# Kernel optimization log

Measured on AMD Instinct MI355X. Metric: run time of the kernel, lower is better.

Reference implementation:

```python
import jax, jax.numpy as jnp
import numpy as np

HIDDEN = 2048
N_HEADS = 16
HEAD_DIM = 128
N_EXPERTS = 8
TOP_K = 2
INTER = 1024
EPS = 1e-5
ROPE_THETA = 10000.0
T = 2048


def rms_norm(x, w, eps=EPS):
    xf = x.astype(jnp.float32)
    return (xf * jax.lax.rsqrt(jnp.mean(xf * xf, axis=-1, keepdims=True) + eps)).astype(x.dtype) * w


def apply_rope(x, positions):
    # x: [T, H, D], NeoX-style half rotation
    d = x.shape[-1]
    inv_freq = 1.0 / (ROPE_THETA ** (jnp.arange(0, d, 2, dtype=jnp.float32) / d))
    ang = positions.astype(jnp.float32)[:, None] * inv_freq  # [T, D/2]
    cos = jnp.cos(ang)[:, None, :]
    sin = jnp.sin(ang)[:, None, :]
    x1, x2 = jnp.split(x, 2, axis=-1)
    return jnp.concatenate([x1 * cos - x2 * sin, x2 * cos + x1 * sin], axis=-1)


def setup_inputs() -> dict:
    key = jax.random.key(0)
    ks = jax.random.split(key, 8)
    s = 0.02
    return {
        "positions": jnp.arange(T, dtype=jnp.int32),
        "hidden_states": jax.random.normal(ks[0], (T, HIDDEN), jnp.float32),
        "qkv_w": jax.random.normal(ks[1], (3 * HIDDEN, HIDDEN), jnp.float32) * s,
        "o_w": jax.random.normal(ks[2], (HIDDEN, HIDDEN), jnp.float32) * s,
        "q_norm_w": jnp.ones((N_HEADS * HEAD_DIM,), jnp.float32),
        "k_norm_w": jnp.ones((N_HEADS * HEAD_DIM,), jnp.float32),
        "post_attn_norm_w": jnp.ones((HIDDEN,), jnp.float32),
        "post_ffn_norm_w": jnp.ones((HIDDEN,), jnp.float32),
        "gate_w": jax.random.normal(ks[3], (N_EXPERTS, HIDDEN), jnp.float32) * s,
        "w_gate": jax.random.normal(ks[4], (N_EXPERTS, INTER, HIDDEN), jnp.float32) * s,
        "w_up": jax.random.normal(ks[5], (N_EXPERTS, INTER, HIDDEN), jnp.float32) * s,
        "w_down": jax.random.normal(ks[6], (N_EXPERTS, HIDDEN, INTER), jnp.float32) * s,
    }


def attention(positions, x, qkv_w, o_w, q_norm_w, k_norm_w):
    qkv = x @ qkv_w.T  # [T, 3*HIDDEN]
    q, k, v = jnp.split(qkv, 3, axis=-1)
    q = rms_norm(q, q_norm_w)  # norm over full flat q dim (FlexOlmo/OLMoE style)
    k = rms_norm(k, k_norm_w)
    q = apply_rope(q.reshape(T, N_HEADS, HEAD_DIM), positions)
    k = apply_rope(k.reshape(T, N_HEADS, HEAD_DIM), positions)
    v = v.reshape(T, N_HEADS, HEAD_DIM)
    scale = 1.0 / np.sqrt(HEAD_DIM)
    scores = jnp.einsum('thd,shd->hts', q, k) * scale
    mask = jnp.tril(jnp.ones((T, T), bool))
    scores = jnp.where(mask[None], scores, -jnp.inf)
    p = jax.nn.softmax(scores, axis=-1)
    out = jnp.einsum('hts,shd->thd', p, v).reshape(T, HIDDEN)
    return out @ o_w.T


def moe(x, gate_w, w_gate, w_up, w_down):
    logits = (x @ gate_w.T).astype(jnp.float32)  # router_logits.float()
    probs = jax.nn.softmax(logits, axis=-1)
    topv, topi = jax.lax.top_k(probs, TOP_K)  # renormalize=False -> use raw softmax weights
    # dense per-expert combine weights: [T, E]
    wdense = jnp.zeros((T, N_EXPERTS), jnp.float32)
    wdense = jnp.sum(jax.nn.one_hot(topi, N_EXPERTS, dtype=jnp.float32) * topv[..., None], axis=1)
    # detach().clone() before dispatch (inference semantics: value unchanged)
    xe = jax.lax.stop_gradient(x)
    g = jnp.einsum('td,efd->tef', xe, w_gate)
    u = jnp.einsum('td,efd->tef', xe, w_up)
    h = jax.nn.silu(g) * u
    y = jnp.einsum('tef,edf->ted', h, w_down)
    return jnp.einsum('ted,te->td', y, wdense)


def reference(positions, hidden_states, qkv_w, o_w, q_norm_w, k_norm_w,
              post_attn_norm_w, post_ffn_norm_w, gate_w, w_gate, w_up, w_down):
    residual = hidden_states
    h = attention(positions, hidden_states, qkv_w, o_w, q_norm_w, k_norm_w)
    h = rms_norm(h, post_attn_norm_w)
    h = h + residual
    residual = h
    h = moe(h, gate_w, w_gate, w_up, w_down)
    h = rms_norm(h, post_ffn_norm_w)
    return residual + h
```

## Files before the change

kernel.cpp:

```cpp
#include <hip/hip_runtime.h>
#include <hip/hip_bf16.h>
#include <cmath>

#define TT 2048
#define HID 2048
#define NHEADS 16
#define HDIM 128
#define NEXP 8
#define INTERD 1024
#define EPSV 1e-5f

typedef short bf16x8 __attribute__((ext_vector_type(8)));
typedef float f32x4 __attribute__((ext_vector_type(4)));

__device__ __forceinline__ unsigned short f2bf(float f) {
    unsigned int u = __builtin_bit_cast(unsigned int, f);
    unsigned int r = (u + 0x7FFFu + ((u >> 16) & 1u)) >> 16;
    return (unsigned short)r;
}
__device__ __forceinline__ float bf2f(unsigned short h) {
    return __builtin_bit_cast(float, (unsigned int)h << 16);
}

__device__ __forceinline__ void gll16(const void* g, void* l) {
    __builtin_amdgcn_global_load_lds((const __attribute__((address_space(1))) void*)g,
                                     (__attribute__((address_space(3))) void*)l, 16, 0, 0);
}

__device__ __forceinline__ float block_reduce_sum_256(float v, float* red) {
    const int tid = threadIdx.x;
    red[tid] = v;
    __syncthreads();
    for (int s = 128; s > 0; s >>= 1) {
        if (tid < s) red[tid] += red[tid + s];
        __syncthreads();
    }
    float r = red[0];
    __syncthreads();
    return r;
}

__global__ __launch_bounds__(256) void split_f32k(const float* __restrict__ x,
                                                  unsigned short* __restrict__ hi,
                                                  unsigned short* __restrict__ lo, int n4) {
    int i = blockIdx.x * 256 + threadIdx.x;
    if (i >= n4) return;
    float4 v = reinterpret_cast<const float4*>(x)[i];
    float xs[4] = {v.x, v.y, v.z, v.w};
    unsigned short hs[4], ls[4];
#pragma unroll
    for (int u = 0; u < 4; ++u) {
        hs[u] = f2bf(xs[u]);
        ls[u] = f2bf(xs[u] - bf2f(hs[u]));
    }
    uint2 hp; hp.x = hs[0] | ((unsigned)hs[1] << 16); hp.y = hs[2] | ((unsigned)hs[3] << 16);
    uint2 lp; lp.x = ls[0] | ((unsigned)ls[1] << 16); lp.y = ls[2] | ((unsigned)ls[3] << 16);
    *reinterpret_cast<uint2*>(hi + (size_t)i * 4) = hp;
    *reinterpret_cast<uint2*>(lo + (size_t)i * 4) = lp;
}

__global__ __launch_bounds__(256) void cvt_bf(const float* __restrict__ x,
                                              unsigned short* __restrict__ y, int n4) {
    int i = blockIdx.x * 256 + threadIdx.x;
    if (i >= n4) return;
    float4 v = reinterpret_cast<const float4*>(x)[i];
    uint2 p;
    p.x = (unsigned)f2bf(v.x) | ((unsigned)f2bf(v.y) << 16);
    p.y = (unsigned)f2bf(v.z) | ((unsigned)f2bf(v.w) << 16);
    *reinterpret_cast<uint2*>(y + (size_t)i * 4) = p;
}

#define GSTAGE(BUF, K0)                                                             \
    {                                                                               \
        char* base_ = (char*)Smem + (BUF) * 32768;                                  \
        _Pragma("unroll")                                                           \
        for (int i_ = 0; i_ < 2; ++i_) {                                            \
            int c_ = tid + i_ * 256;                                                \
            int r_ = c_ >> 2, s_ = c_ & 3;                                          \
            int ko_ = (K0) + (((s_ ^ ((r_ >> 1) & 3)) & 3) << 3);                   \
            gll16(Ah + (size_t)(m0 + r_) * lda + ko_, base_ + c_ * 16);             \
            gll16(Al + (size_t)(m0 + r_) * lda + ko_, base_ + 8192 + c_ * 16);      \
            gll16(Bh + (size_t)(n0 + r_) * K + ko_, base_ + 16384 + c_ * 16);       \
            gll16(Bl + (size_t)(n0 + r_) * K + ko_, base_ + 24576 + c_ * 16);       \
        }                                                                           \
    }

__global__ __launch_bounds__(256) void gemm_sp(const unsigned short* __restrict__ Ah,
                                               const unsigned short* __restrict__ Al,
                                               const unsigned short* __restrict__ Bh,
                                               const unsigned short* __restrict__ Bl,
                                               float* __restrict__ C, int N, int K, int lda) {
    const int nbx = gridDim.x;
    const int nwg = nbx * gridDim.y;
    const int orig = blockIdx.y * nbx + blockIdx.x;
    const int qq = nwg >> 3, rr = nwg & 7;
    const int xcd = orig & 7, loc = orig >> 3;
    const int wgid = (xcd < rr ? xcd * (qq + 1) : rr * (qq + 1) + (xcd - rr) * qq) + loc;
    const int m0 = (wgid / nbx) * 128, n0 = (wgid % nbx) * 128;

    __shared__ __align__(16) unsigned short Smem[2 * 4 * 128 * 32];
    const int tid = threadIdx.x;
    const int w = tid >> 6, l = tid & 63;
    const int lr = l & 15, lg = l >> 4;
    const int wm = w >> 1, wn = w & 1;

    f32x4 acc[4][4];
#pragma unroll
    for (int i = 0; i < 4; ++i)
#pragma unroll
        for (int j = 0; j < 4; ++j) acc[i][j] = f32x4{0.f, 0.f, 0.f, 0.f};

    const int nks = K >> 5;
    GSTAGE(0, 0);
    int cur = 0;
    for (int ks = 0; ks < nks; ++ks) {
        if (ks + 1 < nks) {
            GSTAGE(cur ^ 1, (ks + 1) << 5);
            asm volatile("s_waitcnt vmcnt(8)" ::: "memory");
        } else {
            asm volatile("s_waitcnt vmcnt(0)" ::: "memory");
        }
        __builtin_amdgcn_s_barrier();
        __builtin_amdgcn_sched_barrier(0);
        char* bb = (char*)Smem + cur * 32768;
        bf16x8 bhf[4], blf[4];
#pragma unroll
        for (int nt = 0; nt < 4; ++nt) {
            int row = wn * 64 + nt * 16 + lr;
            int off = row * 64 + (((lg ^ ((row >> 1) & 3)) & 3) << 4);
            bhf[nt] = *reinterpret_cast<const bf16x8*>(bb + 16384 + off);
            blf[nt] = *reinterpret_cast<const bf16x8*>(bb + 24576 + off);
        }
        __builtin_amdgcn_s_setprio(1);
#pragma unroll
        for (int mt = 0; mt < 4; ++mt) {
            int row = wm * 64 + mt * 16 + lr;
            int off = row * 64 + (((lg ^ ((row >> 1) & 3)) & 3) << 4);
            bf16x8 ahf = *reinterpret_cast<const bf16x8*>(bb + off);
            bf16x8 alf = *reinterpret_cast<const bf16x8*>(bb + 8192 + off);
#pragma unroll
            for (int nt = 0; nt < 4; ++nt) {
                acc[mt][nt] = __builtin_amdgcn_mfma_f32_16x16x32_bf16(ahf, bhf[nt], acc[mt][nt], 0, 0, 0);
                acc[mt][nt] = __builtin_amdgcn_mfma_f32_16x16x32_bf16(ahf, blf[nt], acc[mt][nt], 0, 0, 0);
                acc[mt][nt] = __builtin_amdgcn_mfma_f32_16x16x32_bf16(alf, bhf[nt], acc[mt][nt], 0, 0, 0);
            }
        }
        __builtin_amdgcn_s_setprio(0);
        asm volatile("s_waitcnt lgkmcnt(0)" ::: "memory");
        __builtin_amdgcn_s_barrier();
        __builtin_amdgcn_sched_barrier(0);
        cur ^= 1;
    }
#pragma unroll
    for (int mt = 0; mt < 4; ++mt) {
#pragma unroll
        for (int r = 0; r < 4; ++r) {
            size_t crow = (size_t)(m0 + wm * 64 + mt * 16 + lg * 4 + r) * N;
#pragma unroll
            for (int nt = 0; nt < 4; ++nt)
                C[crow + n0 + wn * 64 + nt * 16 + lr] = acc[mt][nt][r];
        }
    }
}

#define GSTAGE_BF(BUF, K0)                                                           \
    {                                                                                \
        char* base_ = sm + (BUF) * 16384;                                            \
        int ko_ = (K0) + x0s;                                                        \
        gll16(A + arow0 * lda + ko_, base_ + tid * 16);                              \
        gll16(A + arow1 * lda + ko_, base_ + (tid + 256) * 16);                      \
        gll16(Bp + brow0 * K + ko_, base_ + 8192 + tid * 16);                        \
        gll16(Bp + brow1 * K + ko_, base_ + 8192 + (tid + 256) * 16);                \
    }

template<int MODE>
__global__ __launch_bounds__(256) void gemm_bf(const unsigned short* __restrict__ A,
                                               const unsigned short* __restrict__ B,
                                               void* __restrict__ Cout,
                                               const float* __restrict__ gsrc,
                                               int N, int K, int lda,
                                               size_t strideB,
                                               const int* __restrict__ gather,
                                               const int* __restrict__ offs,
                                               const int* __restrict__ counts) {
    const int e = blockIdx.z;
    const int cnt = counts[e];
    const int base = offs[e];
    const int m0 = blockIdx.y * 128;
    if (m0 >= cnt) return;
    const int n0 = blockIdx.x * 128;
    const unsigned short* Bp = B + (size_t)e * strideB;

    __shared__ __align__(16) unsigned short Smem[2 * 2 * 128 * 32];
    char* sm = (char*)Smem;
    const int tid = threadIdx.x;
    const int w = tid >> 6, l = tid & 63;
    const int lr = l & 15, lg = l >> 4;
    const int wm = w >> 1, wn = w & 1;

    const int r0 = tid >> 2, s0 = tid & 3;
    const int r1 = r0 + 64;
    const int x0s = ((s0 ^ ((r0 >> 1) & 3)) & 3) << 3;
    const size_t arow0 = (size_t)gather[base + min(m0 + r0, cnt - 1)];
    const size_t arow1 = (size_t)gather[base + min(m0 + r1, cnt - 1)];
    const size_t brow0 = (size_t)(n0 + r0);
    const size_t brow1 = (size_t)(n0 + r1);

    f32x4 acc[4][4];
#pragma unroll
    for (int i = 0; i < 4; ++i)
#pragma unroll
        for (int j = 0; j < 4; ++j) acc[i][j] = f32x4{0.f, 0.f, 0.f, 0.f};

    const int nks = K >> 5;
    GSTAGE_BF(0, 0);
    int cur = 0;
    for (int ks = 0; ks < nks; ++ks) {
        if (ks + 1 < nks) {
            GSTAGE_BF(cur ^ 1, (ks + 1) << 5);
            asm volatile("s_waitcnt vmcnt(4)" ::: "memory");
        } else {
            asm volatile("s_waitcnt vmcnt(0)" ::: "memory");
        }
        __builtin_amdgcn_s_barrier();
        __builtin_amdgcn_sched_barrier(0);
        char* bb = sm + cur * 16384;
        bf16x8 bfr[4];
#pragma unroll
        for (int nt = 0; nt < 4; ++nt) {
            int row = wn * 64 + nt * 16 + lr;
            int off = row * 64 + (((lg ^ ((row >> 1) & 3)) & 3) << 4);
            bfr[nt] = *reinterpret_cast<const bf16x8*>(bb + 8192 + off);
        }
        __builtin_amdgcn_s_setprio(1);
#pragma unroll
        for (int mt = 0; mt < 4; ++mt) {
            int row = wm * 64 + mt * 16 + lr;
            int off = row * 64 + (((lg ^ ((row >> 1) & 3)) & 3) << 4);
            bf16x8 af = *reinterpret_cast<const bf16x8*>(bb + off);
#pragma unroll
            for (int nt = 0; nt < 4; ++nt)
                acc[mt][nt] = __builtin_amdgcn_mfma_f32_16x16x32_bf16(af, bfr[nt], acc[mt][nt], 0, 0, 0);
        }
        __builtin_amdgcn_s_setprio(0);
        asm volatile("s_waitcnt lgkmcnt(0)" ::: "memory");
        __builtin_amdgcn_s_barrier();
        __builtin_amdgcn_sched_barrier(0);
        cur ^= 1;
    }
#pragma unroll
    for (int mt = 0; mt < 4; ++mt) {
#pragma unroll
        for (int r = 0; r < 4; ++r) {
            int rowl = wm * 64 + mt * 16 + lg * 4 + r;
            if (m0 + rowl < cnt) {
                size_t crow = (size_t)(base + m0 + rowl) * N;
#pragma unroll
                for (int nt = 0; nt < 4; ++nt) {
                    size_t idx = crow + n0 + wn * 64 + nt * 16 + lr;
                    if (MODE == 1) {
                        float g = gsrc[idx];
                        ((unsigned short*)Cout)[idx] = f2bf(g / (1.f + expf(-g)) * acc[mt][nt][r]);
                    } else {
                        ((float*)Cout)[idx] = acc[mt][nt][r];
                    }
                }
            }
        }
    }
}

__global__ __launch_bounds__(256) void gemm_moe_down(const unsigned short* __restrict__ Abf,
                                                     const float* __restrict__ B,
                                                     float* __restrict__ C,
                                                     int N, int K, int lda,
                                                     size_t strideB,
                                                     const int* __restrict__ offs,
                                                     const int* __restrict__ counts) {
    const int e = blockIdx.z;
    const int cnt = counts[e];
    const int base = offs[e];
    const int m0 = blockIdx.y * 128;
    if (m0 >= cnt) return;
    const int n0 = blockIdx.x * 128;
    const float* Bp = B + (size_t)e * strideB;

    __shared__ unsigned short smA[128 * 64];
    __shared__ unsigned short smB[128 * 64];
    const int tid = threadIdx.x;
    const int w = tid >> 6, l = tid & 63;
    const int lr = l & 15, lg = l >> 4;
    const int wm = w >> 1, wn = w & 1;
    char* sA = (char*)smA;
    char* sB = (char*)smB;

    f32x4 acc[4][4];
#pragma unroll
    for (int i = 0; i < 4; ++i)
#pragma unroll
        for (int j = 0; j < 4; ++j) acc[i][j] = f32x4{0.f, 0.f, 0.f, 0.f};

    for (int k0 = 0; k0 < K; k0 += 64) {
#pragma unroll
        for (int i = 0; i < 4; ++i) {
            int slot = tid + i * 256;
            int r = slot >> 3, sg = slot & 7;
            int arow = base + min(m0 + r, cnt - 1);
            uint4 v = *reinterpret_cast<const uint4*>(&Abf[(size_t)arow * lda + k0 + sg * 8]);
            *reinterpret_cast<uint4*>(sA + r * 128 + ((sg * 16) ^ ((r & 7) << 4))) = v;
        }
#pragma unroll
        for (int i = 0; i < 8; ++i) {
            int slot = tid + i * 256;
            int r = slot >> 4, kq = slot & 15;
            float4 bv = *reinterpret_cast<const float4*>(&Bp[(size_t)(n0 + r) * K + k0 + kq * 4]);
            uint2 pk;
            pk.x = (unsigned)f2bf(bv.x) | ((unsigned)f2bf(bv.y) << 16);
            pk.y = (unsigned)f2bf(bv.z) | ((unsigned)f2bf(bv.w) << 16);
            *reinterpret_cast<uint2*>(sB + r * 128 + ((kq * 8) ^ ((r & 7) << 4))) = pk;
        }
        __syncthreads();
#pragma unroll
        for (int kk = 0; kk < 2; ++kk) {
            bf16x8 af[4], bfr[4];
#pragma unroll
            for (int mt = 0; mt < 4; ++mt) {
                int row = wm * 64 + mt * 16 + lr;
                af[mt] = *reinterpret_cast<const bf16x8*>(sA + row * 128 + ((kk * 64 + lg * 16) ^ ((row & 7) << 4)));
            }
#pragma unroll
            for (int nt = 0; nt < 4; ++nt) {
                int row = wn * 64 + nt * 16 + lr;
                bfr[nt] = *reinterpret_cast<const bf16x8*>(sB + row * 128 + ((kk * 64 + lg * 16) ^ ((row & 7) << 4)));
            }
#pragma unroll
            for (int mt = 0; mt < 4; ++mt)
#pragma unroll
                for (int nt = 0; nt < 4; ++nt)
                    acc[mt][nt] = __builtin_amdgcn_mfma_f32_16x16x32_bf16(af[mt], bfr[nt], acc[mt][nt], 0, 0, 0);
        }
        __syncthreads();
    }
#pragma unroll
    for (int mt = 0; mt < 4; ++mt) {
#pragma unroll
        for (int r = 0; r < 4; ++r) {
            int rowl = wm * 64 + mt * 16 + lg * 4 + r;
            if (m0 + rowl < cnt) {
                size_t crow = (size_t)(base + m0 + rowl) * N;
#pragma unroll
                for (int nt = 0; nt < 4; ++nt)
                    C[crow + n0 + wn * 64 + nt * 16 + lr] = acc[mt][nt][r];
            }
        }
    }
}

__global__ __launch_bounds__(256) void qknorm_rope_split(float* __restrict__ qkv,
                                                         const float* __restrict__ qw,
                                                         const float* __restrict__ kw,
                                                         const int* __restrict__ pos) {
    __shared__ float xbuf[2048];
    __shared__ float red[256];
    const int t = blockIdx.x, tid = threadIdx.x;
    unsigned short* row16 = (unsigned short*)(qkv + (size_t)t * 6144);
    const float pf = (float)pos[t];
    float vreg[8];
    const float* vsrc = qkv + (size_t)t * 6144 + 4096;
#pragma unroll
    for (int i = 0; i < 8; ++i) vreg[i] = vsrc[tid + i * 256];
    __syncthreads();
#pragma unroll
    for (int i = 0; i < 8; ++i) {
        int d = tid + i * 256;
        unsigned short hi = f2bf(vreg[i]);
        row16[8192 + d] = hi;
        row16[10240 + d] = f2bf(vreg[i] - bf2f(hi));
    }
    for (int part = 0; part < 2; ++part) {
        const float* x = qkv + (size_t)t * 6144 + part * 2048;
        const float* wn = part ? kw : qw;
        const int sbase = part ? 4096 : 0;
        const float outscale = part ? 1.0f : 0.08838834764831845f;
        float s = 0.f;
#pragma unroll
        for (int i = 0; i < 8; ++i) {
            int d = tid + i * 256;
            float v = x[d];
            xbuf[d] = v;
            s = fmaf(v, v, s);
        }
        float tot = block_reduce_sum_256(s, red);
        float scale = rsqrtf(tot * (1.f / HID) + EPSV);
#pragma unroll
        for (int p = tid; p < 1024; p += 256) {
            int hh = p >> 6, j = p & 63;
            int i1 = hh * 128 + j, i2 = i1 + 64;
            float x1 = xbuf[i1] * scale * wn[i1];
            float x2 = xbuf[i2] * scale * wn[i2];
            float invf = expf(-(float)j * 0.14391156831212787f);
            float ang = pf * invf;
            float sn, cs;
            sincosf(ang, &sn, &cs);
            float o1 = (x1 * cs - x2 * sn) * outscale;
            float o2 = (x2 * cs + x1 * sn) * outscale;
            unsigned short h1_ = f2bf(o1);
            row16[sbase + i1] = h1_;
            row16[sbase + 2048 + i1] = f2bf(o1 - bf2f(h1_));
            unsigned short h2_ = f2bf(o2);
            row16[sbase + i2] = h2_;
            row16[sbase + 2048 + i2] = f2bf(o2 - bf2f(h2_));
        }
        __syncthreads();
    }
}

__global__ __launch_bounds__(256) void kvprep(const unsigned short* __restrict__ qkv16,
                                              unsigned short* __restrict__ kt,
                                              unsigned short* __restrict__ vt) {
    const int C = blockIdx.x;
    const int h = blockIdx.y;
    const int tid = threadIdx.x;
#pragma unroll
    for (int p = 0; p < 2; ++p) {
#pragma unroll
        for (int i = 0; i < 4; ++i) {
            int slot = tid + i * 256;
            int r = slot >> 4, sg = slot & 15;
            uint4 v = *reinterpret_cast<const uint4*>(
                qkv16 + (size_t)(C * 64 + r) * 12288 + 4096 + p * 2048 + h * 128 + (sg ^ (r & 7)) * 8);
            *reinterpret_cast<uint4*>(kt + (size_t)(h * 32 + C) * 16384 + p * 8192 + slot * 8) = v;
        }
    }
    __shared__ unsigned short tile[64 * 128];
    char* tb = (char*)tile;
    for (int p = 0; p < 2; ++p) {
#pragma unroll
        for (int i = 0; i < 4; ++i) {
            int c = tid + i * 256;
            int r = c >> 4, dseg = c & 15;
            uint4 v = *reinterpret_cast<const uint4*>(
                qkv16 + (size_t)(C * 64 + r) * 12288 + 8192 + p * 2048 + h * 128 + dseg * 8);
            int swz = dseg ^ (r & 7) ^ (r >> 3);
            *reinterpret_cast<uint4*>(tb + r * 256 + swz * 16) = v;
        }
        __syncthreads();
        unsigned short* ob = vt + (size_t)(h * 32 + C) * 16384 + p * 8192;
#pragma unroll
        for (int i = 0; i < 4; ++i) {
            int c = tid + i * 256;
            int d = c >> 3, j = c & 7;
            unsigned short tmp[8];
#pragma unroll
            for (int u = 0; u < 8; ++u) {
                int s = 8 * j + u;
                int swz = (d >> 3) ^ (s & 7) ^ (s >> 3);
                tmp[u] = *reinterpret_cast<const unsigned short*>(tb + s * 256 + swz * 16 + (d & 7) * 2);
            }
            *reinterpret_cast<uint4*>(ob + (size_t)d * 64 + ((j ^ (d & 7)) * 8)) =
                *reinterpret_cast<const uint4*>(tmp);
        }
        __syncthreads();
    }
}

#define STAGE1(CIDX)                                                                   \
    {                                                                                  \
        const unsigned short* kb_ = kt + (size_t)(h * 32 + (CIDX)) * 16384;            \
        const unsigned short* vb_ = vt + (size_t)(h * 32 + (CIDX)) * 16384;            \
        _Pragma("unroll")                                                              \
        for (int p_ = 0; p_ < 2; ++p_) {                                               \
            _Pragma("unroll")                                                          \
            for (int i_ = 0; i_ < 4; ++i_) {                                           \
                int slot_ = tid + i_ * 256;                                            \
                gll16(kb_ + p_ * 8192 + slot_ * 8, kvb + p_ * 16384 + slot_ * 16);     \
                gll16(vb_ + p_ * 8192 + slot_ * 8, kvb + 32768 + p_ * 16384 + slot_ * 16); \
            }                                                                          \
        }                                                                              \
    }

__global__ __launch_bounds__(256) void attn_mfma(const unsigned short* __restrict__ qkv16,
                                                 const unsigned short* __restrict__ kt,
                                                 const unsigned short* __restrict__ vt,
                                                 unsigned short* __restrict__ oh,
                                                 unsigned short* __restrict__ ol) {
    const int g = blockIdx.x;
    const int rank = (g < 256) ? g : 767 - g;
    const int h = rank & 15;
    const int t0 = (31 - (rank >> 4)) * 64;
    const int tid = threadIdx.x;
    const int w = tid >> 6, l = tid & 63;
    const int lr = l & 15, lg = l >> 4;
    const size_t RS = 12288;
    __shared__ __align__(16) unsigned short KVs[32768];
    __shared__ unsigned short Ps[4][2 * 16 * 64];
    char* kvb = (char*)KVs;
    char* PsB = (char*)(Ps[w]);

    bf16x8 qh[4], ql[4];
    {
        const unsigned short* qp = qkv16 + (size_t)(t0 + w * 16 + lr) * RS + h * 128 + lg * 8;
#pragma unroll
        for (int kk = 0; kk < 4; ++kk) {
            qh[kk] = *reinterpret_cast<const bf16x8*>(qp + kk * 32);
            ql[kk] = *reinterpret_cast<const bf16x8*>(qp + 2048 + kk * 32);
        }
    }
    f32x4 oacc[8];
#pragma unroll
    for (int dt = 0; dt < 8; ++dt) oacc[dt] = f32x4{0.f, 0.f, 0.f, 0.f};
    float mrun[4] = {-INFINITY, -INFINITY, -INFINITY, -INFINITY};
    float lrun[4] = {0.f, 0.f, 0.f, 0.f};

    for (int s0 = 0; s0 <= t0; s0 += 64) {
        STAGE1(s0 >> 6);
        __syncthreads();
        char* KsB = kvb;
        char* VtB = kvb + 32768;

        f32x4 sc[4];
#pragma unroll
        for (int nt = 0; nt < 4; ++nt) sc[nt] = f32x4{0.f, 0.f, 0.f, 0.f};
        __builtin_amdgcn_s_setprio(1);
#pragma unroll
        for (int kk = 0; kk < 4; ++kk) {
#pragma unroll
            for (int nt = 0; nt < 4; ++nt) {
                int row = nt * 16 + lr;
                int off = row * 256 + ((kk * 64 + lg * 16) ^ ((row & 7) << 4));
                bf16x8 kh = *reinterpret_cast<const bf16x8*>(KsB + off);
                bf16x8 kl = *reinterpret_cast<const bf16x8*>(KsB + 16384 + off);
                sc[nt] = __builtin_amdgcn_mfma_f32_16x16x32_bf16(qh[kk], kh, sc[nt], 0, 0, 0);
                sc[nt] = __builtin_amdgcn_mfma_f32_16x16x32_bf16(ql[kk], kh, sc[nt], 0, 0, 0);
                sc[nt] = __builtin_amdgcn_mfma_f32_16x16x32_bf16(qh[kk], kl, sc[nt], 0, 0, 0);
            }
        }
        __builtin_amdgcn_s_setprio(0);
        float mnew[4], alpha[4], psum[4];
#pragma unroll
        for (int r = 0; r < 4; ++r) {
            int row_t = t0 + w * 16 + lg * 4 + r;
            float mx = mrun[r];
#pragma unroll
            for (int nt = 0; nt < 4; ++nt) {
                int col = s0 + nt * 16 + lr;
                float v = sc[nt][r];
                if (col > row_t) v = -INFINITY;
                sc[nt][r] = v;
                mx = fmaxf(mx, v);
            }
#pragma unroll
            for (int o = 1; o < 16; o <<= 1) mx = fmaxf(mx, __shfl_xor(mx, o));
            mnew[r] = mx;
            alpha[r] = expf(mrun[r] - mx);
            mrun[r] = mx;
            psum[r] = 0.f;
        }
#pragma unroll
        for (int nt = 0; nt < 4; ++nt) {
#pragma unroll
            for (int r = 0; r < 4; ++r) {
                float p = expf(sc[nt][r] - mnew[r]);
                psum[r] += p;
                int prow = lg * 4 + r;
                int off = prow * 128 + (((nt * 16 + lr) * 2) ^ ((prow & 7) << 4));
                unsigned short ph = f2bf(p);
                *reinterpret_cast<unsigned short*>(PsB + off) = ph;
                *reinterpret_cast<unsigned short*>(PsB + 2048 + off) = f2bf(p - bf2f(ph));
            }
        }
#pragma unroll
        for (int r = 0; r < 4; ++r) {
            float s = psum[r];
#pragma unroll
            for (int o = 1; o < 16; o <<= 1) s += __shfl_xor(s, o);
            lrun[r] = lrun[r] * alpha[r] + s;
        }
#pragma unroll
        for (int dt = 0; dt < 8; ++dt)
#pragma unroll
            for (int r = 0; r < 4; ++r) oacc[dt][r] *= alpha[r];
        bf16x8 ph[2], pl[2];
#pragma unroll
        for (int kk = 0; kk < 2; ++kk) {
            int off = lr * 128 + ((kk * 64 + lg * 16) ^ ((lr & 7) << 4));
            ph[kk] = *reinterpret_cast<const bf16x8*>(PsB + off);
            pl[kk] = *reinterpret_cast<const bf16x8*>(PsB + 2048 + off);
        }
        __builtin_amdgcn_s_setprio(1);
#pragma unroll
        for (int dt = 0; dt < 8; ++dt) {
            int row = dt * 16 + lr;
#pragma unroll
            for (int kk = 0; kk < 2; ++kk) {
                int off = row * 128 + ((kk * 64 + lg * 16) ^ ((row & 7) << 4));
                bf16x8 vh = *reinterpret_cast<const bf16x8*>(VtB + off);
                bf16x8 vl = *reinterpret_cast<const bf16x8*>(VtB + 16384 + off);
                oacc[dt] = __builtin_amdgcn_mfma_f32_16x16x32_bf16(ph[kk], vh, oacc[dt], 0, 0, 0);
                oacc[dt] = __builtin_amdgcn_mfma_f32_16x16x32_bf16(ph[kk], vl, oacc[dt], 0, 0, 0);
                oacc[dt] = __builtin_amdgcn_mfma_f32_16x16x32_bf16(pl[kk], vh, oacc[dt], 0, 0, 0);
            }
        }
        __builtin_amdgcn_s_setprio(0);
        __syncthreads();
    }
#pragma unroll
    for (int r = 0; r < 4; ++r) {
        float inv = 1.f / lrun[r];
        int row_t = t0 + w * 16 + lg * 4 + r;
#pragma unroll
        for (int dt = 0; dt < 8; ++dt) {
            float o = oacc[dt][r] * inv;
            unsigned short hb = f2bf(o);
            size_t idx = (size_t)row_t * 2048 + h * 128 + dt * 16 + lr;
            oh[idx] = hb;
            ol[idx] = f2bf(o - bf2f(hb));
        }
    }
}

__global__ __launch_bounds__(256) void add_rmsnorm(const float* __restrict__ resid,
                                                   const float* __restrict__ x,
                                                   const float* __restrict__ w,
                                                   float* __restrict__ out,
                                                   unsigned short* __restrict__ outbf) {
    __shared__ float red[256];
    const int t = blockIdx.x, tid = threadIdx.x;
    const float* xr = x + (size_t)t * HID;
    float v[8];
    float s = 0.f;
#pragma unroll
    for (int i = 0; i < 8; ++i) { v[i] = xr[tid + i * 256]; s = fmaf(v[i], v[i], s); }
    float tot = block_reduce_sum_256(s, red);
    float scale = rsqrtf(tot * (1.f / HID) + EPSV);
#pragma unroll
    for (int i = 0; i < 8; ++i) {
        int d = tid + i * 256;
        float o = resid[(size_t)t * HID + d] + v[i] * scale * w[d];
        out[(size_t)t * HID + d] = o;
        outbf[(size_t)t * HID + d] = f2bf(o);
    }
}

__global__ __launch_bounds__(64) void router_kernel(const float* __restrict__ h1,
                                                    const float* __restrict__ gate_w,
                                                    int* __restrict__ topi, float* __restrict__ topv,
                                                    int* __restrict__ slot_tk, int* __restrict__ counts) {
    const int t = blockIdx.x, lane = threadIdx.x;
    float acc[NEXP] = {};
    const float* x = h1 + (size_t)t * HID;
    for (int d = lane; d < HID; d += 64) {
        float xv = x[d];
#pragma unroll
        for (int e = 0; e < NEXP; ++e) acc[e] = fmaf(xv, gate_w[e * HID + d], acc[e]);
    }
#pragma unroll
    for (int e = 0; e < NEXP; ++e)
#pragma unroll
        for (int off = 32; off > 0; off >>= 1) acc[e] += __shfl_down(acc[e], off);
    if (lane == 0) {
        float mx = acc[0];
        for (int e = 1; e < NEXP; ++e) mx = fmaxf(mx, acc[e]);
        float p[NEXP], se = 0.f;
        for (int e = 0; e < NEXP; ++e) { p[e] = expf(acc[e] - mx); se += p[e]; }
        float inv = 1.f / se;
        for (int e = 0; e < NEXP; ++e) p[e] *= inv;
        int e1 = 0;
        for (int e = 1; e < NEXP; ++e) if (p[e] > p[e1]) e1 = e;
        int e2 = (e1 == 0) ? 1 : 0;
        for (int e = 0; e < NEXP; ++e) if (e != e1 && p[e] > p[e2]) e2 = e;
        topi[t * 2] = e1;     topv[t * 2] = p[e1];
        topi[t * 2 + 1] = e2; topv[t * 2 + 1] = p[e2];
        slot_tk[t * 2]     = atomicAdd(&counts[e1], 1);
        slot_tk[t * 2 + 1] = atomicAdd(&counts[e2], 1);
    }
}

__global__ void scan_kernel(const int* __restrict__ counts, int* __restrict__ offs) {
    int o = 0;
    for (int e = 0; e < NEXP; ++e) { offs[e] = o; o += counts[e]; }
}

__global__ __launch_bounds__(256) void map_kernel(const int* __restrict__ topi,
                                                  const int* __restrict__ slot_tk,
                                                  const int* __restrict__ offs,
                                                  int* __restrict__ token_of_row,
                                                  int* __restrict__ row_of_tk) {
    int idx = blockIdx.x * 256 + threadIdx.x;
    if (idx >= TT * 2) return;
    int e = topi[idx];
    int row = offs[e] + slot_tk[idx];
    token_of_row[row] = idx >> 1;
    row_of_tk[idx] = row;
}

__global__ __launch_bounds__(256) void final_combine(const float* __restrict__ h1,
                                                     const float* __restrict__ ypart,
                                                     const float* __restrict__ topv,
                                                     const int* __restrict__ row_of_tk,
                                                     const float* __restrict__ wffn,
                                                     float* __restrict__ out) {
    __shared__ float red[256];
    const int t = blockIdx.x, tid = threadIdx.x;
    const int r0 = row_of_tk[t * 2], r1 = row_of_tk[t * 2 + 1];
    const float w0 = topv[t * 2], w1 = topv[t * 2 + 1];
    const float* y0 = ypart + (size_t)r0 * HID;
    const float* y1 = ypart + (size_t)r1 * HID;
    float v[8];
    float s = 0.f;
#pragma unroll
    for (int i = 0; i < 8; ++i) {
        int d = tid + i * 256;
        v[i] = w0 * y0[d] + w1 * y1[d];
        s = fmaf(v[i], v[i], s);
    }
    float tot = block_reduce_sum_256(s, red);
    float scale = rsqrtf(tot * (1.f / HID) + EPSV);
#pragma unroll
    for (int i = 0; i < 8; ++i) {
        int d = tid + i * 256;
        out[(size_t)t * HID + d] = h1[(size_t)t * HID + d] + v[i] * scale * wffn[d];
    }
}

extern "C" void kernel_launch(void* const* d_in, const int* in_sizes, int n_in,
                              void* d_out, int out_size, void* d_ws, size_t ws_size,
                              hipStream_t stream) {
    const int*   positions = (const int*)d_in[0];
    const float* hidden    = (const float*)d_in[1];
    const float* qkv_w     = (const float*)d_in[2];
    const float* o_w       = (const float*)d_in[3];
    const float* q_norm_w  = (const float*)d_in[4];
    const float* k_norm_w  = (const float*)d_in[5];
    const float* post_attn = (const float*)d_in[6];
    const float* post_ffn  = (const float*)d_in[7];
    const float* gate_w    = (const float*)d_in[8];
    const float* w_gate    = (const float*)d_in[9];
    const float* w_up      = (const float*)d_in[10];
    const float* w_down    = (const float*)d_in[11];
    float* out = (float*)d_out;

    char* ws = (char*)d_ws;
    size_t off = 0;
    auto alloc = [&](size_t bytes) -> void* {
        void* p = ws + off;
        off += (bytes + 255) & ~(size_t)255;
        return p;
    };
    float*          qkvbuf = (float*)alloc((size_t)TT * 6144 * 4);
    unsigned short* hidsp  = (unsigned short*)alloc((size_t)TT * HID * 2 * 2);
    unsigned short* wsp    = (unsigned short*)alloc(((size_t)6144 * HID * 2 + (size_t)HID * HID * 2) * 2);
    float*          h1     = (float*)alloc((size_t)TT * HID * 4);
    unsigned short* h1bf   = (unsigned short*)alloc((size_t)TT * HID * 2);
    int*   topi   = (int*)alloc(TT * 2 * 4);
    float* topv   = (float*)alloc(TT * 2 * 4);
    int*   slot   = (int*)alloc(TT * 2 * 4);
    int*   rowtk  = (int*)alloc(TT * 2 * 4);
    int*   tokrow = (int*)alloc(TT * 2 * 4);
    int*   counts = (int*)alloc(8 * 4);
    int*   offsb  = (int*)alloc(8 * 4);
    if (off > ws_size) return;

    unsigned short* hid_hi   = hidsp;
    unsigned short* hid_lo   = hidsp + (size_t)TT * HID;
    unsigned short* attnO_hi = hid_hi;
    unsigned short* attnO_lo = hid_lo;
    unsigned short* qkvw_hi = wsp;
    unsigned short* qkvw_lo = wsp + (size_t)6144 * HID;
    unsigned short* ow_hi   = wsp + (size_t)2 * 6144 * HID;
    unsigned short* ow_lo   = ow_hi + (size_t)HID * HID;
    unsigned short* vtbuf   = wsp;
    unsigned short* ktbuf   = wsp + (size_t)TT * HID * 2;
    unsigned short* wbfg = wsp;
    unsigned short* wbfu = wsp + (size_t)NEXP * INTERD * HID;
    float*          gbuf   = qkvbuf;
    unsigned short* hinter = (unsigned short*)(qkvbuf + (size_t)4096 * INTERD);
    float*          oOut   = qkvbuf + (size_t)8192 * INTERD;
    float*          ypart  = oOut;

    hipMemsetAsync(counts, 0, 8 * sizeof(int), stream);

    dim3 b256(256);
    split_f32k<<<dim3(TT * HID / 4 / 256), b256, 0, stream>>>(hidden, hid_hi, hid_lo, TT * HID / 4);
    split_f32k<<<dim3(6144 * HID / 4 / 256), b256, 0, stream>>>(qkv_w, qkvw_hi, qkvw_lo, 6144 * HID / 4);
    split_f32k<<<dim3(HID * HID / 4 / 256), b256, 0, stream>>>(o_w, ow_hi, ow_lo, HID * HID / 4);
    gemm_sp<<<dim3(6144 / 128, TT / 128), b256, 0, stream>>>(hid_hi, hid_lo, qkvw_hi, qkvw_lo,
                                                             qkvbuf, 6144, HID, HID);
    qknorm_rope_split<<<dim3(TT), b256, 0, stream>>>(qkvbuf, q_norm_w, k_norm_w, positions);
    kvprep<<<dim3(32, NHEADS), b256, 0, stream>>>((const unsigned short*)qkvbuf, ktbuf, vtbuf);
    attn_mfma<<<dim3(512), b256, 0, stream>>>((const unsigned short*)qkvbuf, ktbuf, vtbuf,
                                              attnO_hi, attnO_lo);
    gemm_sp<<<dim3(HID / 128, TT / 128), b256, 0, stream>>>(attnO_hi, attnO_lo, ow_hi, ow_lo,
                                                            oOut, HID, HID, HID);
    cvt_bf<<<dim3(16384), b256, 0, stream>>>(w_gate, wbfg, NEXP * INTERD * HID / 4);
    cvt_bf<<<dim3(16384), b256, 0, stream>>>(w_up,   wbfu, NEXP * INTERD * HID / 4);
    add_rmsnorm<<<dim3(TT), b256, 0, stream>>>(hidden, oOut, post_attn, h1, h1bf);
    router_kernel<<<dim3(TT), dim3(64), 0, stream>>>(h1, gate_w, topi, topv, slot, counts);
    scan_kernel<<<1, 1, 0, stream>>>(counts, offsb);
    map_kernel<<<dim3((TT * 2 + 255) / 256), b256, 0, stream>>>(topi, slot, offsb, tokrow, rowtk);
    gemm_bf<0><<<dim3(INTERD / 128, 32, NEXP), b256, 0, stream>>>(
        h1bf, wbfg, gbuf, nullptr, INTERD, HID, HID, (size_t)INTERD * HID, tokrow, offsb, counts);
    gemm_bf<1><<<dim3(INTERD / 128, 32, NEXP), b256, 0, stream>>>(
        h1bf, wbfu, hinter, gbuf, INTERD, HID, HID, (size_t)INTERD * HID, tokrow, offsb, counts);
    gemm_moe_down<<<dim3(HID / 128, 32, NEXP), b256, 0, stream>>>(
        hinter, w_down, ypart, HID, INTERD, INTERD, (size_t)HID * INTERD, offsb, counts);
    final_combine<<<dim3(TT), b256, 0, stream>>>(h1, ypart, topv, rowtk, post_ffn, out);
}
```

Before: 717.7 us.

## Fuse gate and up expert GEMMs with in-kernel fp32-to-bf16 weight conversion

New measurement: 733.0 us. 1.02x slower.

```diff
diff --git a/kernel.cpp b/kernel.cpp
--- a/kernel.cpp
+++ b/kernel.cpp
@@ -57,17 +57,6 @@
     uint2 lp; lp.x = ls[0] | ((unsigned)ls[1] << 16); lp.y = ls[2] | ((unsigned)ls[3] << 16);
     *reinterpret_cast<uint2*>(hi + (size_t)i * 4) = hp;
     *reinterpret_cast<uint2*>(lo + (size_t)i * 4) = lp;
-}
-
-__global__ __launch_bounds__(256) void cvt_bf(const float* __restrict__ x,
-                                              unsigned short* __restrict__ y, int n4) {
-    int i = blockIdx.x * 256 + threadIdx.x;
-    if (i >= n4) return;
-    float4 v = reinterpret_cast<const float4*>(x)[i];
-    uint2 p;
-    p.x = (unsigned)f2bf(v.x) | ((unsigned)f2bf(v.y) << 16);
-    p.y = (unsigned)f2bf(v.z) | ((unsigned)f2bf(v.w) << 16);
-    *reinterpret_cast<uint2*>(y + (size_t)i * 4) = p;
 }
 
 #define GSTAGE(BUF, K0)                                                             \
@@ -163,21 +152,10 @@
     }
 }
 
-#define GSTAGE_BF(BUF, K0)                                                           \
-    {                                                                                \
-        char* base_ = sm + (BUF) * 16384;                                            \
-        int ko_ = (K0) + x0s;                                                        \
-        gll16(A + arow0 * lda + ko_, base_ + tid * 16);                              \
-        gll16(A + arow1 * lda + ko_, base_ + (tid + 256) * 16);                      \
-        gll16(Bp + brow0 * K + ko_, base_ + 8192 + tid * 16);                        \
-        gll16(Bp + brow1 * K + ko_, base_ + 8192 + (tid + 256) * 16);                \
-    }
-
-template<int MODE>
-__global__ __launch_bounds__(256) void gemm_bf(const unsigned short* __restrict__ A,
-                                               const unsigned short* __restrict__ B,
-                                               void* __restrict__ Cout,
-                                               const float* __restrict__ gsrc,
+__global__ __launch_bounds__(256) void gemm_gu(const unsigned short* __restrict__ Abf,
+                                               const float* __restrict__ Bg,
+                                               const float* __restrict__ Bu,
+                                               unsigned short* __restrict__ Hout,
                                                int N, int K, int lda,
                                                size_t strideB,
                                                const int* __restrict__ gather,
@@ -189,64 +167,83 @@
     const int m0 = blockIdx.y * 128;
     if (m0 >= cnt) return;
     const int n0 = blockIdx.x * 128;
-    const unsigned short* Bp = B + (size_t)e * strideB;
-
-    __shared__ __align__(16) unsigned short Smem[2 * 2 * 128 * 32];
-    char* sm = (char*)Smem;
+    const float* Bgp = Bg + (size_t)e * strideB;
+    const float* Bup = Bu + (size_t)e * strideB;
+
+    __shared__ unsigned short smA[128 * 64];
+    __shared__ unsigned short smG[128 * 64];
+    __shared__ unsigned short smU[128 * 64];
+    __shared__ int rowsA[128];
     const int tid = threadIdx.x;
+    if (tid < 128) {
+        int rr = min(m0 + tid, cnt - 1);
+        rowsA[tid] = gather[base + rr];
+    }
+    __syncthreads();
+
     const int w = tid >> 6, l = tid & 63;
     const int lr = l & 15, lg = l >> 4;
     const int wm = w >> 1, wn = w & 1;
-
-    const int r0 = tid >> 2, s0 = tid & 3;
-    const int r1 = r0 + 64;
-    const int x0s = ((s0 ^ ((r0 >> 1) & 3)) & 3) << 3;
-    const size_t arow0 = (size_t)gather[base + min(m0 + r0, cnt - 1)];
-    const size_t arow1 = (size_t)gather[base + min(m0 + r1, cnt - 1)];
-    const size_t brow0 = (size_t)(n0 + r0);
-    const size_t brow1 = (size_t)(n0 + r1);
-
-    f32x4 acc[4][4];
+    char* sA = (char*)smA;
+    char* sG = (char*)smG;
+    char* sU = (char*)smU;
+
+    f32x4 accg[4][4], accu[4][4];
 #pragma unroll
     for (int i = 0; i < 4; ++i)
 #pragma unroll
-        for (int j = 0; j < 4; ++j) acc[i][j] = f32x4{0.f, 0.f, 0.f, 0.f};
-
-    const int nks = K >> 5;
-    GSTAGE_BF(0, 0);
-    int cur = 0;
-    for (int ks = 0; ks < nks; ++ks) {
-        if (ks + 1 < nks) {
-            GSTAGE_BF(cur ^ 1, (ks + 1) << 5);
-            asm volatile("s_waitcnt vmcnt(4)" ::: "memory");
-        } else {
-            asm volatile("s_waitcnt vmcnt(0)" ::: "memory");
-        }
-        __builtin_amdgcn_s_barrier();
-        __builtin_amdgcn_sched_barrier(0);
-        char* bb = sm + cur * 16384;
-        bf16x8 bfr[4];
-#pragma unroll
-        for (int nt = 0; nt < 4; ++nt) {
-            int row = wn * 64 + nt * 16 + lr;
-            int off = row * 64 + (((lg ^ ((row >> 1) & 3)) & 3) << 4);
-            bfr[nt] = *reinterpret_cast<const bf16x8*>(bb + 8192 + off);
-        }
-        __builtin_amdgcn_s_setprio(1);
-#pragma unroll
-        for (int mt = 0; mt < 4; ++mt) {
-            int row = wm * 64 + mt * 16 + lr;
-            int off = row * 64 + (((lg ^ ((row >> 1) & 3)) & 3) << 4);
-            bf16x8 af = *reinterpret_cast<const bf16x8*>(bb + off);
-#pragma unroll
-            for (int nt = 0; nt < 4; ++nt)
-                acc[mt][nt] = __builtin_amdgcn_mfma_f32_16x16x32_bf16(af, bfr[nt], acc[mt][nt], 0, 0, 0);
-        }
-        __builtin_amdgcn_s_setprio(0);
-        asm volatile("s_waitcnt lgkmcnt(0)" ::: "memory");
-        __builtin_amdgcn_s_barrier();
-        __builtin_amdgcn_sched_barrier(0);
-        cur ^= 1;
+        for (int j = 0; j < 4; ++j) { accg[i][j] = f32x4{0.f, 0.f, 0.f, 0.f}; accu[i][j] = f32x4{0.f, 0.f, 0.f, 0.f}; }
+
+    for (int k0 = 0; k0 < K; k0 += 64) {
+#pragma unroll
+        for (int i = 0; i < 4; ++i) {
+            int slot = tid + i * 256;
+            int r = slot >> 3, sg = slot & 7;
+            uint4 v = *reinterpret_cast<const uint4*>(&Abf[(size_t)rowsA[r] * lda + k0 + sg * 8]);
+            *reinterpret_cast<uint4*>(sA + r * 128 + ((sg * 16) ^ ((r & 7) << 4))) = v;
+        }
+#pragma unroll
+        for (int i = 0; i < 8; ++i) {
+            int slot = tid + i * 256;
+            int r = slot >> 4, kq = slot & 15;
+            float4 gv = *reinterpret_cast<const float4*>(&Bgp[(size_t)(n0 + r) * K + k0 + kq * 4]);
+            float4 uv = *reinterpret_cast<const float4*>(&Bup[(size_t)(n0 + r) * K + k0 + kq * 4]);
+            uint2 pg, pu;
+            pg.x = (unsigned)f2bf(gv.x) | ((unsigned)f2bf(gv.y) << 16);
+            pg.y = (unsigned)f2bf(gv.z) | ((unsigned)f2bf(gv.w) << 16);
+            pu.x = (unsigned)f2bf(uv.x) | ((unsigned)f2bf(uv.y) << 16);
+            pu.y = (unsigned)f2bf(uv.z) | ((unsigned)f2bf(uv.w) << 16);
+            int off = r * 128 + ((kq * 8) ^ ((r & 7) << 4));
+            *reinterpret_cast<uint2*>(sG + off) = pg;
+            *reinterpret_cast<uint2*>(sU + off) = pu;
+        }
+        __syncthreads();
+#pragma unroll
+        for (int kk = 0; kk < 2; ++kk) {
+            bf16x8 af[4], bgf[4], buf_[4];
+#pragma unroll
+            for (int mt = 0; mt < 4; ++mt) {
+                int row = wm * 64 + mt * 16 + lr;
+                af[mt] = *reinterpret_cast<const bf16x8*>(sA + row * 128 + ((kk * 64 + lg * 16) ^ ((row & 7) << 4)));
+            }
+#pragma unroll
+            for (int nt = 0; nt < 4; ++nt) {
+                int row = wn * 64 + nt * 16 + lr;
+                int off = row * 128 + ((kk * 64 + lg * 16) ^ ((row & 7) << 4));
+                bgf[nt] = *reinterpret_cast<const bf16x8*>(sG + off);
+                buf_[nt] = *reinterpret_cast<const bf16x8*>(sU + off);
+            }
+            __builtin_amdgcn_s_setprio(1);
+#pragma unroll
+            for (int mt = 0; mt < 4; ++mt)
+#pragma unroll
+                for (int nt = 0; nt < 4; ++nt) {
+                    accg[mt][nt] = __builtin_amdgcn_mfma_f32_16x16x32_bf16(af[mt], bgf[nt], accg[mt][nt], 0, 0, 0);
+                    accu[mt][nt] = __builtin_amdgcn_mfma_f32_16x16x32_bf16(af[mt], buf_[nt], accu[mt][nt], 0, 0, 0);
+                }
+            __builtin_amdgcn_s_setprio(0);
+        }
+        __syncthreads();
     }
 #pragma unroll
     for (int mt = 0; mt < 4; ++mt) {
@@ -258,12 +255,9 @@
 #pragma unroll
                 for (int nt = 0; nt < 4; ++nt) {
                     size_t idx = crow + n0 + wn * 64 + nt * 16 + lr;
-                    if (MODE == 1) {
-                        float g = gsrc[idx];
-                        ((unsigned short*)Cout)[idx] = f2bf(g / (1.f + expf(-g)) * acc[mt][nt][r]);
-                    } else {
-                        ((float*)Cout)[idx] = acc[mt][nt][r];
-                    }
+                    float g = accg[mt][nt][r];
+                    float u = accu[mt][nt][r];
+                    Hout[idx] = f2bf(g / (1.f + expf(-g)) * u);
                 }
             }
         }
@@ -771,10 +765,7 @@
     unsigned short* ow_lo   = ow_hi + (size_t)HID * HID;
     unsigned short* vtbuf   = wsp;
     unsigned short* ktbuf   = wsp + (size_t)TT * HID * 2;
-    unsigned short* wbfg = wsp;
-    unsigned short* wbfu = wsp + (size_t)NEXP * INTERD * HID;
-    float*          gbuf   = qkvbuf;
-    unsigned short* hinter = (unsigned short*)(qkvbuf + (size_t)4096 * INTERD);
+    unsigned short* hinter = (unsigned short*)qkvbuf;
     float*          oOut   = qkvbuf + (size_t)8192 * INTERD;
     float*          ypart  = oOut;
 
@@ -792,16 +783,12 @@
                                               attnO_hi, attnO_lo);
     gemm_sp<<<dim3(HID / 128, TT / 128), b256, 0, stream>>>(attnO_hi, attnO_lo, ow_hi, ow_lo,
                                                             oOut, HID, HID, HID);
-    cvt_bf<<<dim3(16384), b256, 0, stream>>>(w_gate, wbfg, NEXP * INTERD * HID / 4);
-    cvt_bf<<<dim3(16384), b256, 0, stream>>>(w_up,   wbfu, NEXP * INTERD * HID / 4);
     add_rmsnorm<<<dim3(TT), b256, 0, stream>>>(hidden, oOut, post_attn, h1, h1bf);
     router_kernel<<<dim3(TT), dim3(64), 0, stream>>>(h1, gate_w, topi, topv, slot, counts);
     scan_kernel<<<1, 1, 0, stream>>>(counts, offsb);
     map_kernel<<<dim3((TT * 2 + 255) / 256), b256, 0, stream>>>(topi, slot, offsb, tokrow, rowtk);
-    gemm_bf<0><<<dim3(INTERD / 128, 32, NEXP), b256, 0, stream>>>(
-        h1bf, wbfg, gbuf, nullptr, INTERD, HID, HID, (size_t)INTERD * HID, tokrow, offsb, counts);
-    gemm_bf<1><<<dim3(INTERD / 128, 32, NEXP), b256, 0, stream>>>(
-        h1bf, wbfu, hinter, gbuf, INTERD, HID, HID, (size_t)INTERD * HID, tokrow, offsb, counts);
+    gemm_gu<<<dim3(INTERD / 128, 32, NEXP), b256, 0, stream>>>(
+        h1bf, w_gate, w_up, hinter, INTERD, HID, HID, (size_t)INTERD * HID, tokrow, offsb, counts);
     gemm_moe_down<<<dim3(HID / 128, 32, NEXP), b256, 0, stream>>>(
         hinter, w_down, ypart, HID, INTERD, INTERD, (size_t)HID * INTERD, offsb, counts);
     final_combine<<<dim3(TT), b256, 0, stream>>>(h1, ypart, topv, rowtk, post_ffn, out);
```
